# Kernel optimization log

Measured on AMD Instinct MI355X. Metric: run time of the kernel, lower is better.

The kernel has to match this reference:

```python
import jax, jax.numpy as jnp
import numpy as np

B, L, C = 4, 2048, 512
H, D = 8, 512          # n_head, hidden_dim (per-head dim)
TEMP = 1.0
EPS = 1e-5


def setup_inputs() -> dict:
    key = jax.random.key(0)
    ks = jax.random.split(key, 12)
    s_in = 1.0 / np.sqrt(C)
    s_out = 1.0 / np.sqrt(H * D)
    return {
        "q": jax.random.normal(ks[0], (B, L, C), jnp.float32),
        "k": jax.random.normal(ks[1], (B, L, C), jnp.float32),
        "v": jax.random.normal(ks[2], (B, L, C), jnp.float32),
        "mask": jax.random.randint(ks[3], (B, L, L), 0, 2).astype(bool),
        "Wq": jax.random.normal(ks[4], (C, H * D), jnp.float32) * s_in,
        "bq": jnp.zeros((H * D,), jnp.float32),
        "Wk": jax.random.normal(ks[5], (C, H * D), jnp.float32) * s_in,
        "bk": jnp.zeros((H * D,), jnp.float32),
        "Wv": jax.random.normal(ks[6], (C, H * D), jnp.float32) * s_in,
        "bv": jnp.zeros((H * D,), jnp.float32),
        "Wo": jax.random.normal(ks[7], (H * D, D), jnp.float32) * s_out,
        "bo": jnp.zeros((D,), jnp.float32),
        "gamma": jnp.ones((D,), jnp.float32),
        "beta": jnp.zeros((D,), jnp.float32),
    }


def reference(q, k, v, mask, Wq, bq, Wk, bk, Wv, bv, Wo, bo, gamma, beta):
    b, ql, _ = q.shape
    residual = q
    qh = (q @ Wq + bq).reshape(b, ql, H, D)           # b,l,h,d
    kh = (k @ Wk + bk).reshape(b, ql, H, D)
    vh = (v @ Wv + bv).reshape(b, ql, H, D)
    # scores in head-major layout to mirror torch permute(2,0,1,3)
    scores = jnp.einsum("bqhd,bkhd->hbqk", qh, kh) / TEMP  # h,b,l,l
    scores = jnp.where(mask[None], -jnp.inf, scores)
    atten = jax.nn.softmax(scores, axis=-1)                 # h,b,l,l
    ctx = jnp.einsum("hbqk,bkhd->bqhd", atten, vh)          # b,l,h,d
    ctx = ctx.reshape(b, ql, H * D)
    out = ctx @ Wo + bo                                     # b,l,D  (dropout in eval mode)
    x = out + residual
    mu = jnp.mean(x, axis=-1, keepdims=True)
    var = jnp.var(x, axis=-1, keepdims=True)
    out = (x - mu) / jnp.sqrt(var + EPS) * gamma + beta
    return out, atten.reshape(H * b, ql, ql)
```

## Files before the change

### kernel.cpp

```cpp
#include <hip/hip_runtime.h>
#include <stdint.h>


typedef unsigned short u16;
typedef _Float16 f16;
typedef __attribute__((ext_vector_type(4))) _Float16 f16x4;
typedef __attribute__((ext_vector_type(8))) _Float16 f16x8;
typedef __attribute__((ext_vector_type(4))) float f32x4;

#define EPI_QKH    0
#define EPI_VHT    1
#define EPI_SCORES 2
#define EPI_CTX    3
#define EPI_OUT    4

__device__ __forceinline__ f32x4 mfma16(f16x8 a, f16x8 b, f32x4 c) {
  return __builtin_amdgcn_mfma_f32_16x16x32_f16(a, b, c, 0, 0, 0);
}

__device__ __forceinline__ void stage_tile_f16(const char* gbase, size_t grow, char* lds, int tid) {
  const int lane = tid & 63, wave = tid >> 6;
#pragma unroll
  for (int c = 0; c < 2; ++c) {
    int chunk = wave * 2 + c;
    int off = chunk * 1024 + lane * 16;
    int r = off >> 6;
    int cb = off & 63;
    const char* g = gbase + (size_t)r * grow + cb;
    __builtin_amdgcn_global_load_lds(
        (__attribute__((address_space(1))) void*)g,
        (__attribute__((address_space(3))) void*)(lds + chunk * 1024),
        16, 0, 0);
  }
}

__device__ __forceinline__ f16x8 load_frag16(const char* lds, int row, int kq) {
  return *(const f16x8*)(lds + ((size_t)row * 32 + kq) * 2);
}

template<int EPI>
__global__ __launch_bounds__(256, 2)
void gemm_k(const char* __restrict__ A, const char* __restrict__ B,
            int lda, int ldb, int K,
            char* __restrict__ C0,
            const float* __restrict__ bias, const float* __restrict__ resid) {
  __shared__ alignas(16) char smem[2][16384];

  const int tid = threadIdx.x, lane = tid & 63, wave = tid >> 6;
  const int wm = wave >> 1, wn = wave & 1;
  const int m0 = blockIdx.x * 128, n0 = blockIdx.y * 128;

  const char* pA = A; const char* pB = B;
  if constexpr (EPI == EPI_SCORES) {
    int z = blockIdx.z, h = z >> 2, b = z & 3;
    size_t e2 = ((size_t)b * 2048 * 4096 + (size_t)h * 512) * 2;
    pA += e2; pB += e2;
  } else if constexpr (EPI == EPI_CTX) {
    int z = blockIdx.z, h = z >> 2, b = z & 3;
    pA += ((size_t)z << 22) * 2;
    pB += ((size_t)(b * 8 + h) * 512 * 2048) * 2;
  }

  f32x4 acc[4][4];
#pragma unroll
  for (int i = 0; i < 4; ++i)
#pragma unroll
    for (int j = 0; j < 4; ++j) acc[i][j] = (f32x4){0.f, 0.f, 0.f, 0.f};

  const size_t rowA = (size_t)lda * 2, rowB = (size_t)ldb * 2;
  const char* gA = pA + (size_t)m0 * rowA;
  const char* gB = pB + (size_t)n0 * rowB;

  const int nk = K >> 5;
  const int kq = (lane >> 4) * 8, l15 = lane & 15, quad = lane >> 4;

  stage_tile_f16(gA, rowA, smem[0], tid);
  stage_tile_f16(gB, rowB, smem[0] + 8192, tid);
  __syncthreads();

  for (int t = 0; t < nk; ++t) {
    char* cur = smem[t & 1];
    if (t + 1 < nk) {
      char* nxt = smem[(t + 1) & 1];
      stage_tile_f16(gA + (size_t)(t + 1) * 64, rowA, nxt, tid);
      stage_tile_f16(gB + (size_t)(t + 1) * 64, rowB, nxt + 8192, tid);
    }

    f16x8 af[4], bf[4];
#pragma unroll
    for (int mi = 0; mi < 4; ++mi)
      af[mi] = load_frag16(cur, wm * 64 + mi * 16 + l15, kq);
#pragma unroll
    for (int ni = 0; ni < 4; ++ni)
      bf[ni] = load_frag16(cur + 8192, wn * 64 + ni * 16 + l15, kq);

#pragma unroll
    for (int mi = 0; mi < 4; ++mi)
#pragma unroll
      for (int ni = 0; ni < 4; ++ni)
        acc[mi][ni] = mfma16(af[mi], bf[ni], acc[mi][ni]);

    __syncthreads();
  }

#pragma unroll
  for (int mi = 0; mi < 4; ++mi)
#pragma unroll
    for (int ni = 0; ni < 4; ++ni)
#pragma unroll
      for (int r = 0; r < 4; ++r) {
        int m = m0 + wm * 64 + mi * 16 + quad * 4 + r;
        int n = n0 + wn * 64 + ni * 16 + l15;
        float v = acc[mi][ni][r];
        if constexpr (EPI == EPI_QKH) {
          v += bias[n];
          ((f16*)C0)[(size_t)m * 4096 + n] = (f16)v;
        } else if constexpr (EPI == EPI_VHT) {
          v += bias[m];
          int hh = m >> 9, d = m & 511, bb = n >> 11, ll = n & 2047;
          ((f16*)C0)[(((size_t)(bb * 8 + hh) * 512 + d) << 11) + ll] = (f16)v;
        } else if constexpr (EPI == EPI_SCORES) {
          int z = blockIdx.z;
          ((float*)C0)[((size_t)z << 22) + ((size_t)m << 11) + n] = v;
        } else if constexpr (EPI == EPI_CTX) {
          int z = blockIdx.z, hh = z >> 2, bb = z & 3;
          ((f16*)C0)[((size_t)(bb * 2048 + m) << 12) + hh * 512 + n] = (f16)v;
        } else {
          v += bias[n] + resid[((size_t)m << 9) + n];
          ((float*)C0)[((size_t)m << 9) + n] = v;
        }
      }
}

__global__ __launch_bounds__(256)
void transpose_cvt_k(const float* __restrict__ in, f16* __restrict__ T,
                     int rows_in, int cols_in) {
  int idx = blockIdx.x * 256 + threadIdx.x;
  if (idx >= rows_in * cols_in) return;
  int c = idx / rows_in, r = idx - c * rows_in;
  T[idx] = (f16)in[(size_t)r * cols_in + c];
}

__global__ __launch_bounds__(256)
void cvt_f16_k(const float* __restrict__ in, f16* __restrict__ out) {
  int i = blockIdx.x * 256 + threadIdx.x;
  float4 v = ((const float4*)in)[i];
  f16x4 h;
  h[0] = (f16)v.x; h[1] = (f16)v.y; h[2] = (f16)v.z; h[3] = (f16)v.w;
  ((f16x4*)out)[i] = h;
}

__global__ __launch_bounds__(256)
void maskprep_k(const int* __restrict__ m32, unsigned char* __restrict__ m8) {
  int i = blockIdx.x * 256 + threadIdx.x;
  int4 v = ((const int4*)m32)[i];
  uchar4 c;
  c.x = (unsigned char)v.x; c.y = (unsigned char)v.y;
  c.z = (unsigned char)v.z; c.w = (unsigned char)v.w;
  ((uchar4*)m8)[i] = c;
}

__global__ __launch_bounds__(256)
void softmax_k(float* __restrict__ att, const unsigned char* __restrict__ m8,
               f16* __restrict__ att16) {
  __shared__ float sm[4];
  int t = threadIdx.x, lane = t & 63, wave = t >> 6;
  size_t r = blockIdx.x;
  int z = (int)(r >> 11), m = (int)(r & 2047), b = z & 3;
  float4* row = (float4*)(att + (r << 11));
  const uchar4* mrow = (const uchar4*)(m8 + (((size_t)b << 22) + ((size_t)m << 11)));
  float4 a = row[t], c = row[t + 256];
  uchar4 ma = mrow[t], mc = mrow[t + 256];
  if (ma.x) a.x = -1e30f; if (ma.y) a.y = -1e30f;
  if (ma.z) a.z = -1e30f; if (ma.w) a.w = -1e30f;
  if (mc.x) c.x = -1e30f; if (mc.y) c.y = -1e30f;
  if (mc.z) c.z = -1e30f; if (mc.w) c.w = -1e30f;
  float mx = fmaxf(fmaxf(fmaxf(a.x, a.y), fmaxf(a.z, a.w)),
                   fmaxf(fmaxf(c.x, c.y), fmaxf(c.z, c.w)));
#pragma unroll
  for (int o = 32; o > 0; o >>= 1) mx = fmaxf(mx, __shfl_xor(mx, o));
  if (lane == 0) sm[wave] = mx;
  __syncthreads();
  mx = fmaxf(fmaxf(sm[0], sm[1]), fmaxf(sm[2], sm[3]));
  a.x = __expf(a.x - mx); a.y = __expf(a.y - mx);
  a.z = __expf(a.z - mx); a.w = __expf(a.w - mx);
  c.x = __expf(c.x - mx); c.y = __expf(c.y - mx);
  c.z = __expf(c.z - mx); c.w = __expf(c.w - mx);
  float s = a.x + a.y + a.z + a.w + c.x + c.y + c.z + c.w;
#pragma unroll
  for (int o = 32; o > 0; o >>= 1) s += __shfl_xor(s, o);
  __syncthreads();
  if (lane == 0) sm[wave] = s;
  __syncthreads();
  s = sm[0] + sm[1] + sm[2] + sm[3];
  float inv = 1.0f / s;
  a.x *= inv; a.y *= inv; a.z *= inv; a.w *= inv;
  c.x *= inv; c.y *= inv; c.z *= inv; c.w *= inv;
  row[t] = a; row[t + 256] = c;
  f16x4* r16 = (f16x4*)(att16 + (r << 11));
  f16x4 ha, hc;
  ha[0] = (f16)a.x; ha[1] = (f16)a.y; ha[2] = (f16)a.z; ha[3] = (f16)a.w;
  hc[0] = (f16)c.x; hc[1] = (f16)c.y; hc[2] = (f16)c.z; hc[3] = (f16)c.w;
  r16[t] = ha; r16[t + 256] = hc;
}

__global__ __launch_bounds__(256)
void ln_k(const float* __restrict__ x, const float* __restrict__ gamma,
          const float* __restrict__ beta, float* __restrict__ out) {
  __shared__ float s1[4], s2[4];
  int t = threadIdx.x, lane = t & 63, wave = t >> 6;
  size_t base = (size_t)blockIdx.x << 9;
  float2 v = ((const float2*)(x + base))[t];
  float s = v.x + v.y;
  float q = v.x * v.x + v.y * v.y;
#pragma unroll
  for (int o = 32; o > 0; o >>= 1) { s += __shfl_xor(s, o); q += __shfl_xor(q, o); }
  if (lane == 0) { s1[wave] = s; s2[wave] = q; }
  __syncthreads();
  s = s1[0] + s1[1] + s1[2] + s1[3];
  q = s2[0] + s2[1] + s2[2] + s2[3];
  float mu = s * (1.0f / 512.0f);
  float var = q * (1.0f / 512.0f) - mu * mu;
  float rs = rsqrtf(var + 1e-5f);
  float2 g = ((const float2*)gamma)[t];
  float2 bb = ((const float2*)beta)[t];
  float2 o2;
  o2.x = (v.x - mu) * rs * g.x + bb.x;
  o2.y = (v.y - mu) * rs * g.y + bb.y;
  ((float2*)(out + base))[t] = o2;
}

extern "C" void kernel_launch(void* const* d_in, const int* in_sizes, int n_in,
                              void* d_out, int out_size, void* d_ws, size_t ws_size,
                              hipStream_t stream) {
  (void)in_sizes; (void)n_in; (void)out_size; (void)ws_size;
  const float* q     = (const float*)d_in[0];
  const float* k     = (const float*)d_in[1];
  const float* v     = (const float*)d_in[2];
  const int*   mask  = (const int*)d_in[3];
  const float* Wq    = (const float*)d_in[4];
  const float* bq    = (const float*)d_in[5];
  const float* Wk    = (const float*)d_in[6];
  const float* bk    = (const float*)d_in[7];
  const float* Wv    = (const float*)d_in[8];
  const float* bv    = (const float*)d_in[9];
  const float* Wo    = (const float*)d_in[10];
  const float* bo    = (const float*)d_in[11];
  const float* gamma = (const float*)d_in[12];
  const float* beta  = (const float*)d_in[13];

  float* out0  = (float*)d_out;
  float* atten = out0 + (size_t)4 * 2048 * 512;

  char* ws = (char*)d_ws;
  const size_t MB = 1024ull * 1024ull;
  f16* WqT  = (f16*)(ws + 0 * MB);
  f16* WkT  = (f16*)(ws + 4 * MB);
  f16* WvT  = (f16*)(ws + 8 * MB);
  f16* WoT  = (f16*)(ws + 12 * MB);
  unsigned char* mask8 = (unsigned char*)(ws + 16 * MB);
  f16* q16  = (f16*)(ws + 32 * MB);
  f16* k16  = (f16*)(ws + 40 * MB);
  f16* v16  = (f16*)(ws + 48 * MB);
  f16* vhT  = (f16*)(ws + 56 * MB);
  f16* atten16 = (f16*)(ws + 120 * MB);
  f16* qh   = (f16*)(ws + 120 * MB);
  f16* kh   = (f16*)(ws + 184 * MB);
  f16* ctx  = (f16*)(ws + 376 * MB);
  float* xbuf = (float*)(ws + 120 * MB);

  transpose_cvt_k<<<8192, 256, 0, stream>>>(Wq, WqT, 512, 4096);
  transpose_cvt_k<<<8192, 256, 0, stream>>>(Wk, WkT, 512, 4096);
  transpose_cvt_k<<<8192, 256, 0, stream>>>(Wv, WvT, 512, 4096);
  transpose_cvt_k<<<8192, 256, 0, stream>>>(Wo, WoT, 4096, 512);
  maskprep_k<<<16384, 256, 0, stream>>>(mask, mask8);
  cvt_f16_k<<<4096, 256, 0, stream>>>(q, q16);
  cvt_f16_k<<<4096, 256, 0, stream>>>(k, k16);
  cvt_f16_k<<<4096, 256, 0, stream>>>(v, v16);

  gemm_k<EPI_QKH><<<dim3(64, 32, 1), 256, 0, stream>>>(
      (const char*)q16, (const char*)WqT, 512, 512, 512, (char*)qh, bq, nullptr);
  gemm_k<EPI_QKH><<<dim3(64, 32, 1), 256, 0, stream>>>(
      (const char*)k16, (const char*)WkT, 512, 512, 512, (char*)kh, bk, nullptr);

  gemm_k<EPI_VHT><<<dim3(32, 64, 1), 256, 0, stream>>>(
      (const char*)WvT, (const char*)v16, 512, 512, 512, (char*)vhT, bv, nullptr);

  gemm_k<EPI_SCORES><<<dim3(16, 16, 32), 256, 0, stream>>>(
      (const char*)qh, (const char*)kh, 4096, 4096, 512, (char*)atten, nullptr, nullptr);

  softmax_k<<<65536, 256, 0, stream>>>(atten, mask8, atten16);

  gemm_k<EPI_CTX><<<dim3(16, 4, 32), 256, 0, stream>>>(
      (const char*)atten16, (const char*)vhT, 2048, 2048, 2048, (char*)ctx, nullptr, nullptr);

  gemm_k<EPI_OUT><<<dim3(64, 4, 1), 256, 0, stream>>>(
      (const char*)ctx, (const char*)WoT, 4096, 4096, 4096, (char*)xbuf, bo, q);

  ln_k<<<8192, 256, 0, stream>>>(xbuf, gamma, beta, out0);
}
```

Measured before the change: 1.563 ms.

## Triple-buffer GEMM pipeline, swizzle block order, split-K output GEMM, tiled weight transpose

The GEMM moves from double to triple buffering, with explicit vmcnt waits, one barrier per k-step and raised wave priority around the MFMA block. Block indices are remapped in groups of 8 to change which tiles run together, aiming at better L2 reuse. The output projection is split over K into two partial buffers that the LayerNorm kernel sums, and the weight transpose now goes through an LDS tile for coalesced accesses. Costs are more LDS per block (48KB, which may lower occupancy) and an extra partial-output buffer that must be written and read back.

Result: no change. 1.535 ms (-1.8%).

```diff
diff --git a/kernel.cpp b/kernel.cpp
--- a/kernel.cpp
+++ b/kernel.cpp
@@ -44,13 +44,19 @@
             int lda, int ldb, int K,
             char* __restrict__ C0,
             const float* __restrict__ bias, const float* __restrict__ resid) {
-  __shared__ alignas(16) char smem[2][16384];
+  __shared__ alignas(16) char smem[3 * 16384];
 
   const int tid = threadIdx.x, lane = tid & 63, wave = tid >> 6;
   const int wm = wave >> 1, wn = wave & 1;
-  const int m0 = blockIdx.x * 128, n0 = blockIdx.y * 128;
+
+  const int nx = gridDim.x, ny = gridDim.y;
+  int id = blockIdx.x + nx * blockIdx.y;
+  const int chunk = (nx * ny) >> 3;
+  id = (id & 7) * chunk + (id >> 3);
+  const int m0 = (id % nx) * 128, n0 = (id / nx) * 128;
 
   const char* pA = A; const char* pB = B;
+  int kz = 0;
   if constexpr (EPI == EPI_SCORES) {
     int z = blockIdx.z, h = z >> 2, b = z & 3;
     size_t e2 = ((size_t)b * 2048 * 4096 + (size_t)h * 512) * 2;
@@ -59,6 +65,10 @@
     int z = blockIdx.z, h = z >> 2, b = z & 3;
     pA += ((size_t)z << 22) * 2;
     pB += ((size_t)(b * 8 + h) * 512 * 2048) * 2;
+  } else if constexpr (EPI == EPI_OUT) {
+    kz = blockIdx.z;
+    pA += (size_t)kz * 2048 * 2;
+    pB += (size_t)kz * 2048 * 2;
   }
 
   f32x4 acc[4][4];
@@ -74,18 +84,27 @@
   const int nk = K >> 5;
   const int kq = (lane >> 4) * 8, l15 = lane & 15, quad = lane >> 4;
 
-  stage_tile_f16(gA, rowA, smem[0], tid);
-  stage_tile_f16(gB, rowB, smem[0] + 8192, tid);
-  __syncthreads();
-
-  for (int t = 0; t < nk; ++t) {
-    char* cur = smem[t & 1];
-    if (t + 1 < nk) {
-      char* nxt = smem[(t + 1) & 1];
-      stage_tile_f16(gA + (size_t)(t + 1) * 64, rowA, nxt, tid);
-      stage_tile_f16(gB + (size_t)(t + 1) * 64, rowB, nxt + 8192, tid);
+  stage_tile_f16(gA, rowA, smem, tid);
+  stage_tile_f16(gB, rowB, smem + 8192, tid);
+  stage_tile_f16(gA + 64, rowA, smem + 16384, tid);
+  stage_tile_f16(gB + 64, rowB, smem + 16384 + 8192, tid);
+
+  int bc = 0;
+  for (int kt = 0; kt < nk; ++kt) {
+    if (kt + 1 < nk) { asm volatile("s_waitcnt vmcnt(4)" ::: "memory"); }
+    else             { asm volatile("s_waitcnt vmcnt(0)" ::: "memory"); }
+    __builtin_amdgcn_sched_barrier(0);
+    __builtin_amdgcn_s_barrier();
+    __builtin_amdgcn_sched_barrier(0);
+
+    if (kt + 2 < nk) {
+      int b2 = bc + 2; if (b2 >= 3) b2 -= 3;
+      char* nb = smem + b2 * 16384;
+      stage_tile_f16(gA + (size_t)(kt + 2) * 64, rowA, nb, tid);
+      stage_tile_f16(gB + (size_t)(kt + 2) * 64, rowB, nb + 8192, tid);
     }
 
+    char* cur = smem + bc * 16384;
     f16x8 af[4], bf[4];
 #pragma unroll
     for (int mi = 0; mi < 4; ++mi)
@@ -94,13 +113,15 @@
     for (int ni = 0; ni < 4; ++ni)
       bf[ni] = load_frag16(cur + 8192, wn * 64 + ni * 16 + l15, kq);
 
+    __builtin_amdgcn_s_setprio(1);
 #pragma unroll
     for (int mi = 0; mi < 4; ++mi)
 #pragma unroll
       for (int ni = 0; ni < 4; ++ni)
         acc[mi][ni] = mfma16(af[mi], bf[ni], acc[mi][ni]);
-
-    __syncthreads();
+    __builtin_amdgcn_s_setprio(0);
+
+    bc = (bc + 1 == 3) ? 0 : bc + 1;
   }
 
 #pragma unroll
@@ -126,19 +147,29 @@
           int z = blockIdx.z, hh = z >> 2, bb = z & 3;
           ((f16*)C0)[((size_t)(bb * 2048 + m) << 12) + hh * 512 + n] = (f16)v;
         } else {
-          v += bias[n] + resid[((size_t)m << 9) + n];
-          ((float*)C0)[((size_t)m << 9) + n] = v;
+          if (kz == 0) v += bias[n] + resid[((size_t)m << 9) + n];
+          ((float*)C0)[(size_t)kz * 8192 * 512 + ((size_t)m << 9) + n] = v;
         }
       }
 }
 
 __global__ __launch_bounds__(256)
 void transpose_cvt_k(const float* __restrict__ in, f16* __restrict__ T,
-                     int rows_in, int cols_in) {
-  int idx = blockIdx.x * 256 + threadIdx.x;
-  if (idx >= rows_in * cols_in) return;
-  int c = idx / rows_in, r = idx - c * rows_in;
-  T[idx] = (f16)in[(size_t)r * cols_in + c];
+                     int R, int Cc) {
+  __shared__ f16 tile[32][33];
+  const int t = threadIdx.x, tc = t & 31, tr = t >> 5;
+  const int bx = blockIdx.x, by = blockIdx.y;
+#pragma unroll
+  for (int k = 0; k < 4; ++k) {
+    int r = by * 32 + tr + k * 8;
+    tile[tr + k * 8][tc] = (f16)in[(size_t)r * Cc + bx * 32 + tc];
+  }
+  __syncthreads();
+#pragma unroll
+  for (int k = 0; k < 4; ++k) {
+    int c = bx * 32 + tr + k * 8;
+    T[(size_t)c * R + by * 32 + tc] = tile[tc][tr + k * 8];
+  }
 }
 
 __global__ __launch_bounds__(256)
@@ -205,12 +236,15 @@
 }
 
 __global__ __launch_bounds__(256)
-void ln_k(const float* __restrict__ x, const float* __restrict__ gamma,
-          const float* __restrict__ beta, float* __restrict__ out) {
+void ln_k(const float* __restrict__ x0, const float* __restrict__ x1,
+          const float* __restrict__ gamma, const float* __restrict__ beta,
+          float* __restrict__ out) {
   __shared__ float s1[4], s2[4];
   int t = threadIdx.x, lane = t & 63, wave = t >> 6;
   size_t base = (size_t)blockIdx.x << 9;
-  float2 v = ((const float2*)(x + base))[t];
+  float2 va = ((const float2*)(x0 + base))[t];
+  float2 vb = ((const float2*)(x1 + base))[t];
+  float2 v; v.x = va.x + vb.x; v.y = va.y + vb.y;
   float s = v.x + v.y;
   float q = v.x * v.x + v.y * v.y;
 #pragma unroll
@@ -269,10 +303,10 @@
   f16* ctx  = (f16*)(ws + 376 * MB);
   float* xbuf = (float*)(ws + 120 * MB);
 
-  transpose_cvt_k<<<8192, 256, 0, stream>>>(Wq, WqT, 512, 4096);
-  transpose_cvt_k<<<8192, 256, 0, stream>>>(Wk, WkT, 512, 4096);
-  transpose_cvt_k<<<8192, 256, 0, stream>>>(Wv, WvT, 512, 4096);
-  transpose_cvt_k<<<8192, 256, 0, stream>>>(Wo, WoT, 4096, 512);
+  transpose_cvt_k<<<dim3(128, 16), 256, 0, stream>>>(Wq, WqT, 512, 4096);
+  transpose_cvt_k<<<dim3(128, 16), 256, 0, stream>>>(Wk, WkT, 512, 4096);
+  transpose_cvt_k<<<dim3(128, 16), 256, 0, stream>>>(Wv, WvT, 512, 4096);
+  transpose_cvt_k<<<dim3(16, 128), 256, 0, stream>>>(Wo, WoT, 4096, 512);
   maskprep_k<<<16384, 256, 0, stream>>>(mask, mask8);
   cvt_f16_k<<<4096, 256, 0, stream>>>(q, q16);
   cvt_f16_k<<<4096, 256, 0, stream>>>(k, k16);
@@ -294,8 +328,8 @@
   gemm_k<EPI_CTX><<<dim3(16, 4, 32), 256, 0, stream>>>(
       (const char*)atten16, (const char*)vhT, 2048, 2048, 2048, (char*)ctx, nullptr, nullptr);
 
-  gemm_k<EPI_OUT><<<dim3(64, 4, 1), 256, 0, stream>>>(
-      (const char*)ctx, (const char*)WoT, 4096, 4096, 4096, (char*)xbuf, bo, q);
-
-  ln_k<<<8192, 256, 0, stream>>>(xbuf, gamma, beta, out0);
-}
+  gemm_k<EPI_OUT><<<dim3(64, 4, 2), 256, 0, stream>>>(
+      (const char*)ctx, (const char*)WoT, 4096, 4096, 2048, (char*)xbuf, bo, q);
+
+  ln_k<<<8192, 256, 0, stream>>>(xbuf, xbuf + (size_t)8192 * 512, gamma, beta, out0);
+}
```
